# Kernel optimization log

Hardware: AMD Instinct MI355X
Metric: run time of the kernel (lower is better)

## Reference

```python
import math
import jax, jax.numpy as jnp
from jax import lax
import numpy as np

TWO_PI = 2.0 * math.pi
CG_ITERS = 30      # DifferentiableLinearSolver(max_iter=30)
CG_TOL = 1e-6
CG_REG = 1e-6      # reg = 1e-6 * I added inside the solver


def build_second_diff_matrix(N, dtype):
    e = jnp.ones(N, dtype)
    e2 = -2.0 * e
    e2 = e2.at[0].set(-1.0).at[-1].set(-1.0)
    oper = jnp.diag(e2) + jnp.diag(e[:-1], -1) + jnp.diag(e[:-1], 1)
    return oper.T @ oper


def cumtrapz(y, dx):
    # cumulative trapezoid along last axis, keeping length (leading zero)
    avg = (y[..., :-1] + y[..., 1:]) * (0.5 * dx)
    c = jnp.cumsum(avg, axis=-1)
    return jnp.concatenate([jnp.zeros_like(y[..., :1]), c], axis=-1)


def differ5(y, delta):
    mid = (y[..., 2:] - y[..., :-2]) / (2.0 * delta)
    first = (y[..., 1:2] - y[..., 0:1]) / delta
    last = (y[..., -1:] - y[..., -2:-1]) / delta
    return jnp.concatenate([first, mid, last], axis=-1)


def projec5(vec, var):
    # per-row norm-ball projection; vec: (B, N)
    M = vec.shape[-1]
    e = jnp.sqrt(M * var)
    n = jnp.linalg.norm(vec, axis=-1, keepdims=True)
    scale = jnp.where(n > e, e / jnp.maximum(n, 1e-30), 1.0)
    return vec * scale


def cg_solve(opedoub, coef, diagv, rhs, x0):
    # Solves (coef*opedoub + diag(diagv) + CG_REG*I) x = rhs via CG,
    # matching torch semantics (early break freezes state).
    def mv(p):
        return coef * (opedoub @ p) + (diagv + CG_REG) * p

    r0 = rhs - mv(x0)
    rs0 = jnp.dot(r0, r0)

    def step(carry, _):
        x, r, p, rsold, done = carry
        Ap = mv(p)
        a = rsold / (jnp.dot(p, Ap) + 1e-12)
        x1 = jnp.where(done, x, x + a * p)
        r1 = jnp.where(done, r, r - a * Ap)
        rsnew = jnp.dot(r1, r1)
        done1 = done | (jnp.sqrt(rsnew) < CG_TOL)
        bta = rsnew / (rsold + 1e-12)
        p1 = jnp.where(done1, p, r1 + bta * p)
        rsold1 = jnp.where(done1, rsold, rsnew)
        return (x1, r1, p1, rsold1, done1), None

    (x, _, _, _, _), _ = lax.scan(step, (x0, r0, r0, rs0, jnp.array(False)), None, length=CG_ITERS)
    return x


def _forward(s, eIF, xm, ym, sum_x, sum_y, lamuda, init_freqs, mode_mask,
             alpha, beta, var, fs, iteration,
             fe_w1, fe_b1, fe_w2, fe_b2,
             pr_w1, pr_b1, pr_w2, pr_b2, pr_w3, pr_b3, iter_weight):
    dtype = s.dtype
    B, N = s.shape
    K = eIF.shape[1]

    # ---- hyperparameter refinement MLP ----
    avg = jnp.mean(init_freqs, axis=1, keepdims=True)              # (B,1)
    h = jax.nn.relu(avg @ fe_w1.T + fe_b1)
    h = jax.nn.relu(h @ fe_w2.T + fe_b2)                            # (B,16)
    cur = jnp.stack([jnp.broadcast_to(alpha, (B,)),
                     jnp.broadcast_to(beta, (B,))], axis=1)         # (B,2)
    z = jnp.concatenate([h, cur], axis=1)                           # (B,18)
    z = jax.nn.relu(z @ pr_w1.T + pr_b1)
    z = jax.nn.relu(z @ pr_w2.T + pr_b2)
    res = jnp.tanh(z @ pr_w3.T + pr_b3)                             # (B,2)
    fac = jax.nn.sigmoid(iter_weight * iteration)
    res = res * fac * 0.1
    new_alpha = jnp.clip(alpha + jnp.mean(res[:, 0] * alpha), 1e-6, 0.01)
    new_beta = jnp.clip(beta + jnp.mean(res[:, 1] * beta), 1e-6, 0.1)

    betathr = jnp.minimum(10.0 ** (iteration / 36.0 - 10.0), new_beta)
    opedoub = build_second_diff_matrix(N, dtype)
    dx = 1.0 / fs

    # Within the torch k-loop, temp sums / lamuda / new_eIF[b,k] all still hold
    # their *input* values, so all (b,k) sub-problems are independent -> vmap.
    u = projec5(s - sum_x - sum_y - lamuda / new_alpha, var)        # (B,N)

    phase = TWO_PI * cumtrapz(eIF, dx)                               # (B,K,N)
    cosm = jnp.cos(phase)
    sinm = jnp.sin(phase)
    resid = (s[:, None, :] - (sum_x[:, None, :] - xm * cosm)
             - (sum_y[:, None, :] - ym * sinm)
             - u[:, None, :] - (lamuda / new_alpha)[:, None, :])
    rhs_x = cosm * resid
    rhs_y = sinm * resid

    coefA = 2.0 / new_alpha
    flat = lambda t: t.reshape(B * K, N)
    cg_v = jax.vmap(cg_solve, in_axes=(None, None, 0, 0, 0))

    xs = cg_v(opedoub, coefA, flat(cosm ** 2), flat(rhs_x), flat(xm)).reshape(B, K, N)
    ys = cg_v(opedoub, coefA, flat(sinm ** 2), flat(rhs_y), flat(ym)).reshape(B, K, N)

    xbar = differ5(xs, dx)
    ybar = differ5(ys, dx)
    denom = xs ** 2 + ys ** 2 + 1e-12
    deltaIF = (xs * ybar - ys * xbar) / (denom * TWO_PI)

    coefS = 2.0 / betathr
    ones_d = jnp.ones((B * K, N), dtype)
    zeros_d = jnp.zeros((B * K, N), dtype)
    smooth = cg_v(opedoub, coefS, ones_d, flat(deltaIF), zeros_d).reshape(B, K, N)
    eIF_s = eIF - 0.5 * smooth

    active = (mode_mask != 0)[:, :, None]                            # (B,K,1)
    new_xm = jnp.where(active, xs, xm)
    new_ym = jnp.where(active, ys, ym)
    new_eIF = jnp.where(active, eIF_s, eIF)

    new_phase = TWO_PI * cumtrapz(new_eIF, dx)
    maskf = active.astype(dtype)
    bsx = jnp.sum(maskf * new_xm * jnp.cos(new_phase), axis=1)       # (B,N)
    bsy = jnp.sum(maskf * new_ym * jnp.sin(new_phase), axis=1)
    new_lamuda = lamuda + new_alpha * (u + bsx + bsy - s)

    return (new_eIF, new_xm, new_ym, bsx, bsy, new_lamuda, new_alpha, new_beta)


def setup_inputs() -> dict:
    key = jax.random.key(0)
    B, K, N = 8, 4, 2048
    ks = jax.random.split(key, 20)
    f32 = jnp.float32
    inp = {
        "s": jax.random.normal(ks[0], (B, N), f32),
        "eIF": 50.0 + 200.0 * jax.random.uniform(ks[1], (B, K, N), f32),
        "xm": 0.1 * jax.random.normal(ks[2], (B, K, N), f32),
        "ym": 0.1 * jax.random.normal(ks[3], (B, K, N), f32),
        "sum_x": 0.1 * jax.random.normal(ks[4], (B, N), f32),
        "sum_y": 0.1 * jax.random.normal(ks[5], (B, N), f32),
        "lamuda": 0.01 * jax.random.normal(ks[6], (B, N), f32),
        "init_freqs": 50.0 + 200.0 * jax.random.uniform(ks[7], (B, K), f32),
        "mode_mask": jnp.ones((B, K), jnp.int32),
        "alpha": jnp.asarray(0.005, f32),
        "beta": jnp.asarray(0.05, f32),
        "var": jnp.asarray(0.01, f32),
        "fs": jnp.asarray(2000.0, f32),
        "iteration": 1,
        # HyperparameterRefinement params (torch Linear: y = x @ W.T + b)
        "fe_w1": 0.1 * jax.random.normal(ks[8], (32, 1), f32),
        "fe_b1": jnp.zeros((32,), f32),
        "fe_w2": 0.1 * jax.random.normal(ks[9], (16, 32), f32),
        "fe_b2": jnp.zeros((16,), f32),
        "pr_w1": 0.1 * jax.random.normal(ks[10], (64, 18), f32),
        "pr_b1": jnp.zeros((64,), f32),
        "pr_w2": 0.1 * jax.random.normal(ks[11], (32, 64), f32),
        "pr_b2": jnp.zeros((32,), f32),
        "pr_w3": 0.1 * jax.random.normal(ks[12], (2, 32), f32),
        "pr_b3": jnp.zeros((2,), f32),
        "iter_weight": jnp.asarray(0.1, f32),
    }
    return inp


def reference(s, eIF, xm, ym, sum_x, sum_y, lamuda, init_freqs, mode_mask,
              alpha, beta, var, fs, iteration,
              fe_w1, fe_b1, fe_w2, fe_b2,
              pr_w1, pr_b1, pr_w2, pr_b2, pr_w3, pr_b3, iter_weight):
    return _forward(s, eIF, xm, ym, sum_x, sum_y, lamuda, init_freqs, mode_mask,
                    alpha, beta, var, fs, iteration,
                    fe_w1, fe_b1, fe_w2, fe_b2,
                    pr_w1, pr_b1, pr_w2, pr_b2, pr_w3, pr_b3, iter_weight)
```

## Files before the change

kernel.cpp:

```cpp
#include <hip/hip_runtime.h>
#include <math.h>

#define Nq 2048
#define Bq 8
#define Kq 4
#define BKq 32
#define NL 32
#define NP 16
#define TWO_PI_D 6.283185307179586
#define PI_D 3.141592653589793
#define INV2PI_D 0.15915494309189535

typedef float v2f __attribute__((ext_vector_type(2)));

__device__ __forceinline__ v2f mk2(float a, float b) {
  v2f r; r.x = a; r.y = b; return r;
}


__device__ __forceinline__ double wave_sum_d(double v) {
#pragma unroll
  for (int off = 1; off < 64; off <<= 1) v += __shfl_xor(v, off, 64);
  return v;
}

__device__ __forceinline__ float dpp_sum_f32(float v) {
  v += __int_as_float(__builtin_amdgcn_update_dpp(0, __float_as_int(v), 0x111, 0xf, 0xf, false));
  v += __int_as_float(__builtin_amdgcn_update_dpp(0, __float_as_int(v), 0x112, 0xf, 0xf, false));
  v += __int_as_float(__builtin_amdgcn_update_dpp(0, __float_as_int(v), 0x114, 0xf, 0xe, false));
  v += __int_as_float(__builtin_amdgcn_update_dpp(0, __float_as_int(v), 0x118, 0xf, 0xc, false));
  v += __int_as_float(__builtin_amdgcn_update_dpp(0, __float_as_int(v), 0x142, 0xa, 0xf, false));
  v += __int_as_float(__builtin_amdgcn_update_dpp(0, __float_as_int(v), 0x143, 0xc, 0xf, false));
  return __int_as_float(__builtin_amdgcn_readlane(__float_as_int(v), 63));
}

__device__ __forceinline__ float dpp_shr1(float v) {
  return __int_as_float(__builtin_amdgcn_update_dpp(0, __float_as_int(v), 0x138, 0xf, 0xf, false));
}
__device__ __forceinline__ float dpp_shl1(float v) {
  return __int_as_float(__builtin_amdgcn_update_dpp(0, __float_as_int(v), 0x130, 0xf, 0xf, false));
}

__device__ __forceinline__ double lane_excl_prefix_d(double T, int lane) {
  double acc = T;
#pragma unroll
  for (int off = 1; off < 64; off <<= 1) {
    double t = __shfl_up(acc, off, 64);
    if (lane >= off) acc += t;
  }
  return acc - T;
}

__device__ __forceinline__ void fast_sincos_rev(double hrev, float* sn, float* cs) {
  double k = trunc(hrev);
  float rv = (float)(hrev - k);
  *sn = __builtin_amdgcn_sinf(rv);
  *cs = __builtin_amdgcn_cosf(rv);
}

template <bool UNIT_DIAG, bool ZERO_X0>
__device__ __forceinline__ void cg_wave_pk(float coef, const v2f* De, float deu,
                                           v2f* R, v2f* X, int lane) {
  v2f P[NP], AP[NP];

  auto applyA = [&](const v2f* V) {
    float lm2 = dpp_shr1(V[NP - 1].x);
    float lm1 = dpp_shr1(V[NP - 1].y);
    float rp1 = dpp_shl1(V[0].x);
    float rp2 = dpp_shl1(V[0].y);
    v2f Vm = mk2(lm2, lm1);
    v2f Vp = mk2(rp1, rp2);
    v2f S[NP], Sm;
    Sm = Vm + V[0];
#pragma unroll
    for (int j = 0; j < NP - 1; ++j) S[j] = V[j] + V[j + 1];
    S[NP - 1] = V[NP - 1] + Vp;
#pragma unroll
    for (int j = 0; j < NP; ++j) {
      v2f Vprev = (j == 0) ? Vm : V[j - 1];
      v2f Vnext = (j == NP - 1) ? Vp : V[j + 1];
      v2f t = Vprev + Vnext;
      t += V[j] * 6.0f;
      float m1x = (j == 0) ? Sm.y : S[j - 1].y;
      float m1y = S[j].x;
      t.x -= 4.0f * m1x;
      t.y -= 4.0f * m1y;
      v2f de = UNIT_DIAG ? mk2(deu, deu) : De[j];
      AP[j] = t * coef + de * V[j];
    }
    if (lane == 0) {
      AP[0].x += coef * (V[0].y - 4.0f * V[0].x);
      AP[0].y += coef * V[0].x;
    }
    if (lane == 63) {
      AP[NP - 1].x += coef * V[NP - 1].y;
      AP[NP - 1].y += coef * (V[NP - 1].x - 4.0f * V[NP - 1].y);
    }
  };

  float rsold, inv_rsold;
  {
    if (!ZERO_X0) {
      applyA(X);
#pragma unroll
      for (int j = 0; j < NP; ++j) R[j] -= AP[j];
    }
    v2f a0 = mk2(0.f, 0.f), a1 = mk2(0.f, 0.f);
#pragma unroll
    for (int j = 0; j < NP; j += 2) {
      P[j] = R[j];
      a0 += R[j] * R[j];
      P[j + 1] = R[j + 1];
      a1 += R[j + 1] * R[j + 1];
    }
    v2f s = a0 + a1;
    rsold = dpp_sum_f32(s.x + s.y);
    inv_rsold = __builtin_amdgcn_rcpf(rsold + 1e-12f);
  }

  for (int it = 0; it < 30; ++it) {
    applyA(P);
    v2f a0 = mk2(0.f, 0.f), a1 = mk2(0.f, 0.f);
#pragma unroll
    for (int j = 0; j < NP; j += 2) {
      a0 += P[j] * AP[j];
      a1 += P[j + 1] * AP[j + 1];
    }
    v2f s = a0 + a1;
    float pap = dpp_sum_f32(s.x + s.y);
    float a = rsold * __builtin_amdgcn_rcpf(pap + 1e-12f);
    v2f r0 = mk2(0.f, 0.f), r1 = mk2(0.f, 0.f);
#pragma unroll
    for (int j = 0; j < NP; j += 2) {
      X[j] += P[j] * a;
      R[j] -= AP[j] * a;
      r0 += R[j] * R[j];
      X[j + 1] += P[j + 1] * a;
      R[j + 1] -= AP[j + 1] * a;
      r1 += R[j + 1] * R[j + 1];
    }
    v2f t = r0 + r1;
    float rsnew = dpp_sum_f32(t.x + t.y);
    if (rsnew < 1e-12f) break;
    float bta = rsnew * inv_rsold;
#pragma unroll
    for (int j = 0; j < NP; ++j) P[j] = R[j] + P[j] * bta;
    rsold = rsnew;
    inv_rsold = __builtin_amdgcn_rcpf(rsnew + 1e-12f);
  }
}

__global__ __launch_bounds__(128, 1) void row_kernel(
    const float* __restrict__ s, const float* __restrict__ eIF,
    const float* __restrict__ xm, const float* __restrict__ ym,
    const float* __restrict__ sum_x, const float* __restrict__ sum_y,
    const float* __restrict__ lamuda, const float* __restrict__ init_freqs,
    const int* __restrict__ mode_mask, const float* __restrict__ alpha_p,
    const float* __restrict__ beta_p, const float* __restrict__ var_p,
    const float* __restrict__ fs_p, const int* __restrict__ iter_p,
    const float* __restrict__ fe_w1, const float* __restrict__ fe_b1,
    const float* __restrict__ fe_w2, const float* __restrict__ fe_b2,
    const float* __restrict__ pr_w1, const float* __restrict__ pr_b1,
    const float* __restrict__ pr_w2, const float* __restrict__ pr_b2,
    const float* __restrict__ pr_w3, const float* __restrict__ pr_b3,
    const float* __restrict__ iter_w_p, double* __restrict__ hdr,
    float* __restrict__ out_eIF, float* __restrict__ out_xm,
    float* __restrict__ out_ym, float* __restrict__ cx_w,
    float* __restrict__ cy_w, float* __restrict__ out_scal) {
  __shared__ double sh_avg[Bq];
  __shared__ double sh_h1[Bq][32];
  __shared__ double sh_z[Bq][18];
  __shared__ double sh_z1[Bq][64];
  __shared__ double sh_z2[Bq][32];
  __shared__ double sh_res[Bq][2];
  __shared__ double sh_hdr[6];
  __shared__ float sh_xs[Nq], sh_ys[Nq];

  const int tid = threadIdx.x;
  const int wv = tid >> 6, lane = tid & 63;
  const int row = blockIdx.x, b = row >> 2;
  const int bb = b * Nq, base = row * Nq;

  double alpha = (double)alpha_p[0], beta = (double)beta_p[0];
  double iterv = (double)iter_p[0];
  if (tid < Bq) {
    double avg = 0.0;
#pragma unroll
    for (int k = 0; k < Kq; ++k) avg += (double)init_freqs[tid * Kq + k];
    sh_avg[tid] = avg * (1.0 / Kq);
  }
  __syncthreads();
  for (int n = tid; n < 256; n += 128) {
    int b2 = n >> 5, j = n & 31;
    double v = (double)fe_w1[j] * sh_avg[b2] + (double)fe_b1[j];
    sh_h1[b2][j] = v > 0.0 ? v : 0.0;
  }
  __syncthreads();
  {
    int b2 = tid >> 4, j = tid & 15;
    double acc = (double)fe_b2[j];
    for (int i = 0; i < 32; ++i) acc += (double)fe_w2[j * 32 + i] * sh_h1[b2][i];
    sh_z[b2][j] = acc > 0.0 ? acc : 0.0;
  }
  if (tid < Bq) {
    sh_z[tid][16] = alpha;
    sh_z[tid][17] = beta;
  }
  __syncthreads();
  for (int n = tid; n < 512; n += 128) {
    int b2 = n >> 6, j = n & 63;
    double acc = (double)pr_b1[j];
    for (int i = 0; i < 18; ++i) acc += (double)pr_w1[j * 18 + i] * sh_z[b2][i];
    sh_z1[b2][j] = acc > 0.0 ? acc : 0.0;
  }
  __syncthreads();
  for (int n = tid; n < 256; n += 128) {
    int b2 = n >> 5, j = n & 31;
    double acc = (double)pr_b2[j];
    for (int i = 0; i < 64; ++i) acc += (double)pr_w2[j * 64 + i] * sh_z1[b2][i];
    sh_z2[b2][j] = acc > 0.0 ? acc : 0.0;
  }
  __syncthreads();
  if (tid < 16) {
    int b2 = tid >> 1, c = tid & 1;
    double acc = (double)pr_b3[c];
    for (int i = 0; i < 32; ++i) acc += (double)pr_w3[c * 32 + i] * sh_z2[b2][i];
    double fac = 1.0 / (1.0 + exp(-(double)iter_w_p[0] * iterv));
    sh_res[b2][c] = tanh(acc) * fac * 0.1;
  }
  __syncthreads();
  if (tid == 0) {
    double r0 = 0.0, r1 = 0.0;
    for (int q = 0; q < Bq; ++q) { r0 += sh_res[q][0]; r1 += sh_res[q][1]; }
    double na = fmin(fmax(alpha + r0 * alpha * (1.0 / Bq), 1e-6), 0.01);
    double nb = fmin(fmax(beta + r1 * beta * (1.0 / Bq), 1e-6), 0.1);
    double betathr = fmin(pow(10.0, iterv / 36.0 - 10.0), nb);
    sh_hdr[0] = na;
    sh_hdr[1] = 2.0 / na;
    sh_hdr[2] = 2.0 / betathr;
    sh_hdr[3] = 1.0 / na;
    hdr[0] = na;
    hdr[4] = 1.0 / na;
    out_scal[0] = (float)na;
    out_scal[1] = (float)nb;
  }
  __syncthreads();
  const float coefA = (float)sh_hdr[1];
  const float coefS = (float)sh_hdr[2];
  const double inva = sh_hdr[3];

  double tv[NL];
  {
    const float4* S4 = reinterpret_cast<const float4*>(s + bb);
    const float4* SX4 = reinterpret_cast<const float4*>(sum_x + bb);
    const float4* SY4 = reinterpret_cast<const float4*>(sum_y + bb);
    const float4* L4 = reinterpret_cast<const float4*>(lamuda + bb);
    double n0 = 0.0, n1 = 0.0;
#pragma unroll
    for (int q = 0; q < 8; ++q) {
      float4 av = S4[lane * 8 + q];
      float4 bv = SX4[lane * 8 + q];
      float4 cv = SY4[lane * 8 + q];
      float4 dv = L4[lane * 8 + q];
      int e = 4 * q;
      tv[e + 0] = (double)av.x - (double)bv.x - (double)cv.x - (double)dv.x * inva;
      tv[e + 1] = (double)av.y - (double)bv.y - (double)cv.y - (double)dv.y * inva;
      tv[e + 2] = (double)av.z - (double)bv.z - (double)cv.z - (double)dv.z * inva;
      tv[e + 3] = (double)av.w - (double)bv.w - (double)cv.w - (double)dv.w * inva;
      n0 += tv[e + 0] * tv[e + 0];
      n1 += tv[e + 1] * tv[e + 1];
      n0 += tv[e + 2] * tv[e + 2];
      n1 += tv[e + 3] * tv[e + 3];
    }
    double nsq = wave_sum_d(n0 + n1);
    double nn = sqrt(nsq);
    double ee = sqrt((double)Nq * (double)var_p[0]);
    double scale = (nn > ee) ? ee / fmax(nn, 1e-30) : 1.0;
    if (tid == 0 && (row & 3) == 0) hdr[8 + b] = scale;
    double oms = 1.0 - scale;
#pragma unroll
    for (int e = 0; e < NL; ++e) tv[e] *= oms;
  }

  const double fsv = (double)fs_p[0];
  const double hdx = 0.5 / fsv;
  v2f De[NP], R[NP], X[NP];
  {
    double ev[NL], pl[NL];
    const float4* E4 = reinterpret_cast<const float4*>(eIF + base);
#pragma unroll
    for (int q = 0; q < 8; ++q) {
      float4 e4 = E4[lane * 8 + q];
      ev[4 * q + 0] = (double)e4.x;
      ev[4 * q + 1] = (double)e4.y;
      ev[4 * q + 2] = (double)e4.z;
      ev[4 * q + 3] = (double)e4.w;
    }
    pl[0] = ev[0];
#pragma unroll
    for (int e = 1; e < NL; ++e) pl[e] = pl[e - 1] + ev[e];
    double offs = lane_excl_prefix_d(pl[NL - 1], lane);
    double y0 = __shfl(ev[0], 0, 64);
    const float4* XM4 = reinterpret_cast<const float4*>(xm + base);
    const float4* YM4 = reinterpret_cast<const float4*>(ym + base);
#pragma unroll
    for (int q = 0; q < 8; ++q) {
      float4 xm4 = XM4[lane * 8 + q];
      float4 ym4 = YM4[lane * 8 + q];
      float xa[4] = {xm4.x, xm4.y, xm4.z, xm4.w};
      float ya[4] = {ym4.x, ym4.y, ym4.z, ym4.w};
#pragma unroll
      for (int t2 = 0; t2 < 4; ++t2) {
        int e = 4 * q + t2;
        double hrev = hdx * (2.0 * (offs + pl[e]) - ev[e] - y0);
        float sn, cs;
        fast_sincos_rev(hrev, &sn, &cs);
        float xmv = xa[t2], ymv = ya[t2];
        double resid = tv[e] + (double)xmv * (double)cs + (double)ymv * (double)sn;
        float trig = (wv == 0) ? cs : sn;
        float de = trig * trig + 1e-6f;
        float rr = (float)((double)trig * resid);
        float xx = (wv == 0) ? xmv : ymv;
        int j = e >> 1;
        if (e & 1) {
          De[j].y = de; R[j].y = rr; X[j].y = xx;
        } else {
          De[j].x = de; R[j].x = rr; X[j].x = xx;
        }
      }
    }
  }

  cg_wave_pk<false, false>(coefA, De, 0.0f, R, X, lane);

  {
    float* dst = (wv == 0) ? sh_xs : sh_ys;
#pragma unroll
    for (int e = 0; e < NL; ++e) {
      float xv = (e & 1) ? X[e >> 1].y : X[e >> 1].x;
      dst[e * 64 + lane] = xv;
    }
  }
  __syncthreads();

  {
    float xs[NL], ys[NL];
#pragma unroll
    for (int e = 0; e < NL; ++e) {
      xs[e] = sh_xs[e * 64 + lane];
      ys[e] = sh_ys[e * 64 + lane];
    }
    float invdx = (float)fsv, inv2dx = 0.5f * invdx;
    float xl = dpp_shr1(xs[NL - 1]), xr = dpp_shl1(xs[0]);
    float yl = dpp_shr1(ys[NL - 1]), yr = dpp_shl1(ys[0]);
#pragma unroll
    for (int e = 0; e < NL; ++e) {
      int i = lane * NL + e;
      float xm1 = (e >= 1) ? xs[e - 1] : xl;
      float xp1 = (e <= NL - 2) ? xs[e + 1] : xr;
      float ym1 = (e >= 1) ? ys[e - 1] : yl;
      float yp1 = (e <= NL - 2) ? ys[e + 1] : yr;
      float xb, yb;
      if (i == 0) {
        xb = (xp1 - xs[e]) * invdx;
        yb = (yp1 - ys[e]) * invdx;
      } else if (i == Nq - 1) {
        xb = (xs[e] - xm1) * invdx;
        yb = (ys[e] - ym1) * invdx;
      } else {
        xb = (xp1 - xm1) * inv2dx;
        yb = (yp1 - ym1) * inv2dx;
      }
      float denom = xs[e] * xs[e] + ys[e] * ys[e] + 1e-12f;
      float rr = (xs[e] * yb - ys[e] * xb) / (denom * (float)TWO_PI_D);
      int j = e >> 1;
      if (e & 1) {
        R[j].y = rr; X[j].y = 0.0f;
      } else {
        R[j].x = rr; X[j].x = 0.0f;
      }
    }
  }

  cg_wave_pk<true, true>(coefS, nullptr, 1.0f + 1e-6f, R, X, lane);

  bool active = mode_mask[row] != 0;
  double eifn[NL], pl[NL];
#pragma unroll
  for (int e = 0; e < NL; ++e) {
    int i = base + lane * NL + e;
    double eifv = (double)eIF[i];
    double sm = (double)((e & 1) ? X[e >> 1].y : X[e >> 1].x);
    eifn[e] = active ? (eifv - 0.5 * sm) : eifv;
  }
  if (wv == 0) {
#pragma unroll
    for (int e = 0; e < NL; ++e) {
      int i = base + lane * NL + e;
      out_eIF[i] = (float)eifn[e];
      out_xm[i] = active ? sh_xs[e * 64 + lane] : xm[i];
    }
  } else {
#pragma unroll
    for (int e = 0; e < NL; ++e) {
      int i = base + lane * NL + e;
      out_ym[i] = active ? sh_ys[e * 64 + lane] : ym[i];
    }
  }
  pl[0] = eifn[0];
#pragma unroll
  for (int e = 1; e < NL; ++e) pl[e] = pl[e - 1] + eifn[e];
  double offs = lane_excl_prefix_d(pl[NL - 1], lane);
  double y0 = __shfl(eifn[0], 0, 64);
#pragma unroll
  for (int e = 0; e < NL; ++e) {
    int i = base + lane * NL + e;
    double hrev = hdx * (2.0 * (offs + pl[e]) - eifn[e] - y0);
    float sn, cs;
    fast_sincos_rev(hrev, &sn, &cs);
    if (wv == 0)
      cx_w[i] = active ? sh_xs[e * 64 + lane] * cs : 0.0f;
    else
      cy_w[i] = active ? sh_ys[e * 64 + lane] * sn : 0.0f;
  }
}

__global__ __launch_bounds__(128) void final_kernel(
    const float* __restrict__ s, const float* __restrict__ sum_x,
    const float* __restrict__ sum_y, const float* __restrict__ lamuda,
    const double* __restrict__ hdr, const float* __restrict__ cx_w,
    const float* __restrict__ cy_w, float* __restrict__ out_bsx,
    float* __restrict__ out_bsy, float* __restrict__ out_lam) {
  int gi = blockIdx.x * 128 + threadIdx.x;
  int b = gi >> 11, i = gi & (Nq - 1);
  double na = hdr[0], inva = hdr[4], scale = hdr[8 + b];
  double sv = (double)s[gi];
  double t = sv - (double)sum_x[gi] - (double)sum_y[gi] -
             (double)lamuda[gi] * inva;
  double bx = 0.0, by = 0.0;
#pragma unroll
  for (int k = 0; k < Kq; ++k) {
    bx += (double)cx_w[(b * Kq + k) * Nq + i];
    by += (double)cy_w[(b * Kq + k) * Nq + i];
  }
  double u = t * scale;
  double nl = (double)lamuda[gi] + na * (u + bx + by - sv);
  out_bsx[gi] = (float)bx;
  out_bsy[gi] = (float)by;
  out_lam[gi] = (float)nl;
}

extern "C" void kernel_launch(void* const* d_in, const int* in_sizes, int n_in,
                              void* d_out, int out_size, void* d_ws, size_t ws_size,
                              hipStream_t stream) {
  (void)in_sizes; (void)n_in; (void)out_size; (void)ws_size;
  const float* s = (const float*)d_in[0];
  const float* eIF = (const float*)d_in[1];
  const float* xm = (const float*)d_in[2];
  const float* ym = (const float*)d_in[3];
  const float* sum_x = (const float*)d_in[4];
  const float* sum_y = (const float*)d_in[5];
  const float* lamuda = (const float*)d_in[6];
  const float* init_freqs = (const float*)d_in[7];
  const int* mode_mask = (const int*)d_in[8];
  const float* alpha = (const float*)d_in[9];
  const float* beta = (const float*)d_in[10];
  const float* var = (const float*)d_in[11];
  const float* fs = (const float*)d_in[12];
  const int* iteration = (const int*)d_in[13];
  const float* fe_w1 = (const float*)d_in[14];
  const float* fe_b1 = (const float*)d_in[15];
  const float* fe_w2 = (const float*)d_in[16];
  const float* fe_b2 = (const float*)d_in[17];
  const float* pr_w1 = (const float*)d_in[18];
  const float* pr_b1 = (const float*)d_in[19];
  const float* pr_w2 = (const float*)d_in[20];
  const float* pr_b2 = (const float*)d_in[21];
  const float* pr_w3 = (const float*)d_in[22];
  const float* pr_b3 = (const float*)d_in[23];
  const float* iter_weight = (const float*)d_in[24];

  float* out = (float*)d_out;
  const int BN = Bq * Nq;
  const int BKN = BKq * Nq;
  float* out_eIF = out;
  float* out_xm = out + BKN;
  float* out_ym = out + 2 * BKN;
  float* out_bsx = out + 3 * BKN;
  float* out_bsy = out + 3 * BKN + BN;
  float* out_lam = out + 3 * BKN + 2 * BN;
  float* out_scal = out + 3 * BKN + 3 * BN;

  double* W = (double*)d_ws;
  double* hdr = W;
  float* F = (float*)(W + 16);
  float* cx_w = F;
  float* cy_w = F + BKN;

  row_kernel<<<BKq, 128, 0, stream>>>(
      s, eIF, xm, ym, sum_x, sum_y, lamuda, init_freqs, mode_mask, alpha, beta,
      var, fs, iteration, fe_w1, fe_b1, fe_w2, fe_b2, pr_w1, pr_b1, pr_w2,
      pr_b2, pr_w3, pr_b3, iter_weight, hdr, out_eIF, out_xm, out_ym, cx_w,
      cy_w, out_scal);
  final_kernel<<<BN / 128, 128, 0, stream>>>(s, sum_x, sum_y, lamuda, hdr,
                                             cx_w, cy_w, out_bsx, out_bsy,
                                             out_lam);
}
```

Measured before the change: 155.7 us.

## Fuse final reduction into row kernel via per-batch atomic counter

```diff
diff --git a/kernel.cpp b/kernel.cpp
--- a/kernel.cpp
+++ b/kernel.cpp
@@ -163,10 +163,12 @@
     const float* __restrict__ pr_w1, const float* __restrict__ pr_b1,
     const float* __restrict__ pr_w2, const float* __restrict__ pr_b2,
     const float* __restrict__ pr_w3, const float* __restrict__ pr_b3,
-    const float* __restrict__ iter_w_p, double* __restrict__ hdr,
+    const float* __restrict__ iter_w_p, int* __restrict__ cnt,
     float* __restrict__ out_eIF, float* __restrict__ out_xm,
     float* __restrict__ out_ym, float* __restrict__ cx_w,
-    float* __restrict__ cy_w, float* __restrict__ out_scal) {
+    float* __restrict__ cy_w, float* __restrict__ out_scal,
+    float* __restrict__ out_bsx, float* __restrict__ out_bsy,
+    float* __restrict__ out_lam) {
   __shared__ double sh_avg[Bq];
   __shared__ double sh_h1[Bq][32];
   __shared__ double sh_z[Bq][18];
@@ -239,8 +241,6 @@
     sh_hdr[1] = 2.0 / na;
     sh_hdr[2] = 2.0 / betathr;
     sh_hdr[3] = 1.0 / na;
-    hdr[0] = na;
-    hdr[4] = 1.0 / na;
     out_scal[0] = (float)na;
     out_scal[1] = (float)nb;
   }
@@ -250,6 +250,7 @@
   const double inva = sh_hdr[3];
 
   double tv[NL];
+  double scale_d;
   {
     const float4* S4 = reinterpret_cast<const float4*>(s + bb);
     const float4* SX4 = reinterpret_cast<const float4*>(sum_x + bb);
@@ -275,9 +276,8 @@
     double nsq = wave_sum_d(n0 + n1);
     double nn = sqrt(nsq);
     double ee = sqrt((double)Nq * (double)var_p[0]);
-    double scale = (nn > ee) ? ee / fmax(nn, 1e-30) : 1.0;
-    if (tid == 0 && (row & 3) == 0) hdr[8 + b] = scale;
-    double oms = 1.0 - scale;
+    scale_d = (nn > ee) ? ee / fmax(nn, 1e-30) : 1.0;
+    double oms = 1.0 - scale_d;
 #pragma unroll
     for (int e = 0; e < NL; ++e) tv[e] *= oms;
   }
@@ -423,31 +423,73 @@
     else
       cy_w[i] = active ? sh_ys[e * 64 + lane] * sn : 0.0f;
   }
-}
-
-__global__ __launch_bounds__(128) void final_kernel(
-    const float* __restrict__ s, const float* __restrict__ sum_x,
-    const float* __restrict__ sum_y, const float* __restrict__ lamuda,
-    const double* __restrict__ hdr, const float* __restrict__ cx_w,
-    const float* __restrict__ cy_w, float* __restrict__ out_bsx,
-    float* __restrict__ out_bsy, float* __restrict__ out_lam) {
-  int gi = blockIdx.x * 128 + threadIdx.x;
-  int b = gi >> 11, i = gi & (Nq - 1);
-  double na = hdr[0], inva = hdr[4], scale = hdr[8 + b];
-  double sv = (double)s[gi];
-  double t = sv - (double)sum_x[gi] - (double)sum_y[gi] -
-             (double)lamuda[gi] * inva;
-  double bx = 0.0, by = 0.0;
-#pragma unroll
-  for (int k = 0; k < Kq; ++k) {
-    bx += (double)cx_w[(b * Kq + k) * Nq + i];
-    by += (double)cy_w[(b * Kq + k) * Nq + i];
-  }
-  double u = t * scale;
-  double nl = (double)lamuda[gi] + na * (u + bx + by - sv);
-  out_bsx[gi] = (float)bx;
-  out_bsy[gi] = (float)by;
-  out_lam[gi] = (float)nl;
+
+  __threadfence();
+  __syncthreads();
+  if (tid == 0) atomicAdd(&cnt[b], 1);
+
+  if ((row & 3) != 0) return;
+
+  if (tid == 0) {
+    while (__hip_atomic_load(&cnt[b], __ATOMIC_RELAXED,
+                             __HIP_MEMORY_SCOPE_AGENT) < Kq) {
+      __builtin_amdgcn_s_sleep(1);
+    }
+    __threadfence();
+  }
+  __syncthreads();
+
+  {
+    const double na_d = sh_hdr[0];
+    const float4* S4f = reinterpret_cast<const float4*>(s + bb);
+    const float4* SX4f = reinterpret_cast<const float4*>(sum_x + bb);
+    const float4* SY4f = reinterpret_cast<const float4*>(sum_y + bb);
+    const float4* L4f = reinterpret_cast<const float4*>(lamuda + bb);
+    float4* BSX4 = reinterpret_cast<float4*>(out_bsx + bb);
+    float4* BSY4 = reinterpret_cast<float4*>(out_bsy + bb);
+    float4* LAM4 = reinterpret_cast<float4*>(out_lam + bb);
+#pragma unroll
+    for (int q = 0; q < 4; ++q) {
+      int idx4 = tid * 4 + q;
+      float4 sv4 = S4f[idx4];
+      float4 sx4 = SX4f[idx4];
+      float4 sy4 = SY4f[idx4];
+      float4 lv4 = L4f[idx4];
+      double bx0 = 0.0, bx1 = 0.0, bx2 = 0.0, bx3 = 0.0;
+      double by0 = 0.0, by1 = 0.0, by2 = 0.0, by3 = 0.0;
+#pragma unroll
+      for (int k = 0; k < Kq; ++k) {
+        float4 cx4 = reinterpret_cast<const float4*>(cx_w + (b * Kq + k) * Nq)[idx4];
+        float4 cy4 = reinterpret_cast<const float4*>(cy_w + (b * Kq + k) * Nq)[idx4];
+        bx0 += (double)cx4.x; bx1 += (double)cx4.y;
+        bx2 += (double)cx4.z; bx3 += (double)cx4.w;
+        by0 += (double)cy4.x; by1 += (double)cy4.y;
+        by2 += (double)cy4.z; by3 += (double)cy4.w;
+      }
+      double sv[4] = {(double)sv4.x, (double)sv4.y, (double)sv4.z, (double)sv4.w};
+      double sx[4] = {(double)sx4.x, (double)sx4.y, (double)sx4.z, (double)sx4.w};
+      double sy[4] = {(double)sy4.x, (double)sy4.y, (double)sy4.z, (double)sy4.w};
+      double lv[4] = {(double)lv4.x, (double)lv4.y, (double)lv4.z, (double)lv4.w};
+      double bxa[4] = {bx0, bx1, bx2, bx3};
+      double bya[4] = {by0, by1, by2, by3};
+      float4 obx, oby, olam;
+      float* obxp = &obx.x;
+      float* obyp = &oby.x;
+      float* olap = &olam.x;
+#pragma unroll
+      for (int c = 0; c < 4; ++c) {
+        double t = sv[c] - sx[c] - sy[c] - lv[c] * inva;
+        double u = t * scale_d;
+        double nl = lv[c] + na_d * (u + bxa[c] + bya[c] - sv[c]);
+        obxp[c] = (float)bxa[c];
+        obyp[c] = (float)bya[c];
+        olap[c] = (float)nl;
+      }
+      BSX4[idx4] = obx;
+      BSY4[idx4] = oby;
+      LAM4[idx4] = olam;
+    }
+  }
 }
 
 extern "C" void kernel_launch(void* const* d_in, const int* in_sizes, int n_in,
@@ -491,18 +533,15 @@
   float* out_lam = out + 3 * BKN + 2 * BN;
   float* out_scal = out + 3 * BKN + 3 * BN;
 
-  double* W = (double*)d_ws;
-  double* hdr = W;
-  float* F = (float*)(W + 16);
+  int* cnt = (int*)d_ws;
+  float* F = (float*)((char*)d_ws + 128);
   float* cx_w = F;
   float* cy_w = F + BKN;
 
+  hipMemsetAsync(cnt, 0, 128, stream);
   row_kernel<<<BKq, 128, 0, stream>>>(
       s, eIF, xm, ym, sum_x, sum_y, lamuda, init_freqs, mode_mask, alpha, beta,
       var, fs, iteration, fe_w1, fe_b1, fe_w2, fe_b2, pr_w1, pr_b1, pr_w2,
-      pr_b2, pr_w3, pr_b3, iter_weight, hdr, out_eIF, out_xm, out_ym, cx_w,
-      cy_w, out_scal);
-  final_kernel<<<BN / 128, 128, 0, stream>>>(s, sum_x, sum_y, lamuda, hdr,
-                                             cx_w, cy_w, out_bsx, out_bsy,
-                                             out_lam);
-}
+      pr_b2, pr_w3, pr_b3, iter_weight, cnt, out_eIF, out_xm, out_ym, cx_w,
+      cy_w, out_scal, out_bsx, out_bsy, out_lam);
+}
```

Result: slower. 164.4 us (+5.5%).
